# Optimization experiments

Measured on AMD Instinct MI355X. Metric: run time of the kernel, lower is better.

## Reference

```python
import jax, jax.numpy as jnp
import numpy as np

NUM_HEADS = 8
HEAD_DIM = 64  # hidden_size 512 / 8 heads


def setup_inputs() -> dict:
    key = jax.random.key(0)
    ks = jax.random.split(key, 9)
    B, S, D, H = 64, 512, 512, 512  # batch, feat_num, input_size, hidden_size
    s = 0.02
    return {
        "x": jax.random.normal(ks[0], (B, S, D), dtype=jnp.float32),
        "wq": jax.random.normal(ks[1], (D, H), dtype=jnp.float32) * s,
        "bq": jax.random.normal(ks[2], (H,), dtype=jnp.float32) * s,
        "wk": jax.random.normal(ks[3], (D, H), dtype=jnp.float32) * s,
        "bk": jax.random.normal(ks[4], (H,), dtype=jnp.float32) * s,
        "wv": jax.random.normal(ks[5], (D, H), dtype=jnp.float32) * s,
        "bv": jax.random.normal(ks[6], (H,), dtype=jnp.float32) * s,
        "wo": jax.random.normal(ks[7], (H, D), dtype=jnp.float32) * s,
        "bo": jax.random.normal(ks[8], (D,), dtype=jnp.float32) * s,
    }


def reference(x, wq, bq, wk, bk, wv, bv, wo, bo):
    B, S, D = x.shape
    # QKV projections -> [B, heads, S, head_dim]
    def split_heads(t):
        return t.reshape(B, S, NUM_HEADS, HEAD_DIM).transpose(0, 2, 1, 3)
    q = split_heads(x @ wq + bq)
    k = split_heads(x @ wk + bk)
    v = split_heads(x @ wv + bv)
    # attention: [B, h, S, S]
    scores = jnp.einsum("bhsd,bhtd->bhst", q, k) / jnp.sqrt(
        jnp.asarray(HEAD_DIM, dtype=x.dtype)
    )
    probs = jax.nn.softmax(scores, axis=-1)  # dropout p=0 -> identity
    ctx = jnp.einsum("bhst,bhtd->bhsd", probs, v)
    ctx = ctx.transpose(0, 2, 1, 3).reshape(B, S, NUM_HEADS * HEAD_DIM)
    # output dense + residual + relu (dropout identity)
    out = jax.nn.relu(x + (ctx @ wo + bo))
    return out
```

## Files before the change

kernel.cpp:

```cpp
#include <hip/hip_runtime.h>
#include <hip/hip_bf16.h>

typedef unsigned short u16;
typedef unsigned int u32;
typedef __attribute__((ext_vector_type(8))) short short8;
typedef __attribute__((ext_vector_type(4))) float f32x4;
typedef __attribute__((ext_vector_type(4))) _Float16 f16x4;

static __device__ __forceinline__ u16 f2b(float f) {
  unsigned u = __builtin_bit_cast(unsigned, f);
  unsigned r = u + 0x7fffu + ((u >> 16) & 1u);
  return (u16)(r >> 16);
}
static __device__ __forceinline__ float b2f(u16 v) {
  return __builtin_bit_cast(float, (u32)v << 16);
}
static __device__ __forceinline__ unsigned pk2(float a, float b) {
  return (unsigned)f2b(a) | ((unsigned)f2b(b) << 16);
}
static __device__ __forceinline__ u32 pkh(float a, float b) {
  return __builtin_bit_cast(u32, __builtin_amdgcn_cvt_pkrtz(a, b));
}

static __device__ __forceinline__ void gl_lds16(const u16* g, u16* l) {
  __builtin_amdgcn_global_load_lds(
      (const __attribute__((address_space(1))) unsigned*)g,
      (__attribute__((address_space(3))) unsigned*)l, 16, 0, 0);
}


__global__ __launch_bounds__(256) void prep(
    const float* __restrict__ wq, const float* __restrict__ wk,
    const float* __restrict__ wv, const float* __restrict__ wo,
    const float* __restrict__ x, u16* __restrict__ wqkv_t,
    u16* __restrict__ wo_t, u16* __restrict__ xb) {
  int t = blockIdx.x * 256 + threadIdx.x;
  if (t < 786432) {
    int n = t >> 9, k = t & 511;
    const float* w = (n < 512) ? wq : (n < 1024 ? wk : wv);
    wqkv_t[(size_t)n * 512 + k] = f2b(w[k * 512 + (n & 511)]);
  } else if (t < 1048576) {
    int j = t - 786432;
    int n = j >> 9, k = j & 511;
    wo_t[(size_t)n * 512 + k] = f2b(wo[k * 512 + n]);
  } else {
    size_t i = (size_t)(t - 1048576) * 4;
    float4 v = *reinterpret_cast<const float4*>(&x[i]);
    uint2 p;
    p.x = pk2(v.x, v.y);
    p.y = pk2(v.z, v.w);
    *reinterpret_cast<uint2*>(&xb[i]) = p;
  }
}

__global__ __launch_bounds__(256, 4) void gemm_qkv(
    const u16* __restrict__ xb, const u16* __restrict__ wt,
    const float* __restrict__ bq, const float* __restrict__ bk,
    const float* __restrict__ bv, u16* __restrict__ qkv) {
  __shared__ u16 As[128 * 64];
  __shared__ u16 Bs[128 * 64];
  const int tid = threadIdx.x;
  const int wave = tid >> 6, lane = tid & 63;
  const int wm = wave & 1, wn = wave >> 1;
  const int lr = lane & 15, lg = lane >> 4;
  const int id = blockIdx.x;
  const int xcd = id & 7, s = id >> 3;
  const int n0 = (s % 12) * 128;
  const int m0 = ((s / 12) * 8 + xcd) * 128;

  const f32x4 fz = {0.f, 0.f, 0.f, 0.f};
  f32x4 acc[4][4];
#pragma unroll
  for (int i = 0; i < 4; ++i)
#pragma unroll
    for (int j = 0; j < 4; ++j) acc[i][j] = fz;

  for (int kb = 0; kb < 512; kb += 64) {
#pragma unroll
    for (int j = 0; j < 4; ++j) {
      const int cb = (wave * 4 + j) * 64;
      const int c = cb + lane;
      const int r = c >> 3;
      const int cg = (c & 7) ^ (r & 7);
      gl_lds16(&xb[(size_t)(m0 + r) * 512 + kb + (cg << 3)], &As[cb * 8]);
      gl_lds16(&wt[(size_t)(n0 + r) * 512 + kb + (cg << 3)], &Bs[cb * 8]);
    }
    __syncthreads();
#pragma unroll
    for (int ks = 0; ks < 2; ++ks) {
      short8 af[4], bb[4];
#pragma unroll
      for (int i = 0; i < 4; ++i)
        af[i] = *reinterpret_cast<const short8*>(
            &As[(wm * 64 + i * 16 + lr) * 64 +
                (((ks * 4 + lg) ^ (lr & 7)) << 3)]);
#pragma unroll
      for (int j = 0; j < 4; ++j)
        bb[j] = *reinterpret_cast<const short8*>(
            &Bs[(wn * 64 + j * 16 + lr) * 64 +
                (((ks * 4 + lg) ^ (lr & 7)) << 3)]);
#pragma unroll
      for (int i = 0; i < 4; ++i)
#pragma unroll
        for (int j = 0; j < 4; ++j)
          acc[i][j] = __builtin_amdgcn_mfma_f32_16x16x32_bf16(
              af[i], bb[j], acc[i][j], 0, 0, 0);
    }
    __syncthreads();
  }
#pragma unroll
  for (int i = 0; i < 4; ++i) {
    const int row0 = m0 + wm * 64 + i * 16 + lg * 4;
#pragma unroll
    for (int j = 0; j < 4; ++j) {
      const int col = n0 + wn * 64 + j * 16 + lr;
      const float bias =
          (col < 512) ? bq[col] : (col < 1024 ? bk[col - 512] : bv[col - 1024]);
#pragma unroll
      for (int r = 0; r < 4; ++r) {
        float v = acc[i][j][r] + bias;
        u16 ov;
        if (col < 512)
          ov = f2b(v * 0.125f);
        else if (col < 1024)
          ov = f2b(v);
        else
          ov = __builtin_bit_cast(u16, (_Float16)v);
        qkv[(size_t)(row0 + r) * 1536 + col] = ov;
      }
    }
  }
}

__global__ __launch_bounds__(256, 3) void attn(u16* __restrict__ qkv) {
  __shared__ u16 QOs[128 * 66];
  __shared__ u16 Ks[2][64 * 64];
  __shared__ u16 VsT[2][64 * 70];

  const int tid = threadIdx.x;
  const int wave = tid >> 6, lane = tid & 63;
  const int lr = lane & 15, lg = lane >> 4;
  const int bx = blockIdx.x;
  const int xcd = bx & 7, s = bx >> 3;
  const int q0 = (s & 3) * 128;
  const int bh = (s >> 2) * 8 + xcd;
  const int b = bh >> 3, h = bh & 7;
  const size_t rowbase = (size_t)b * 512;

#pragma unroll
  for (int j = 0; j < 4; ++j) {
    const int cb = (wave * 4 + j) * 64, c = cb + lane;
    const int r = c >> 3, cg = (c & 7) ^ (r & 7);
    gl_lds16(&qkv[(rowbase + q0 + r) * 1536 + h * 64 + (cg << 3)],
             &QOs[cb * 8]);
  }
#pragma unroll
  for (int j = 0; j < 2; ++j) {
    const int cb = (wave * 2 + j) * 64, c = cb + lane;
    const int r = c >> 3, cg = (c & 7) ^ (r & 7);
    gl_lds16(&qkv[(rowbase + r) * 1536 + 512 + h * 64 + (cg << 3)],
             &Ks[0][cb * 8]);
  }
  uint4 vreg[2];
#pragma unroll
  for (int i = 0; i < 2; ++i) {
    int idx = tid + i * 256, r = idx >> 3, cg = idx & 7;
    vreg[i] = *reinterpret_cast<const uint4*>(
        &qkv[(rowbase + r) * 1536 + 1024 + h * 64 + cg * 8]);
  }
#pragma unroll
  for (int i = 0; i < 2; ++i) {
    int idx = tid + i * 256, r = idx >> 3, cg = idx & 7;
    const u16* pv = reinterpret_cast<const u16*>(&vreg[i]);
#pragma unroll
    for (int jj = 0; jj < 8; ++jj) VsT[0][(cg * 8 + jj) * 70 + r] = pv[jj];
  }
  __syncthreads();

  short8 aq[2][2];
#pragma unroll
  for (int g = 0; g < 2; ++g)
#pragma unroll
    for (int ks = 0; ks < 2; ++ks)
      aq[g][ks] = *reinterpret_cast<const short8*>(
          &QOs[(wave * 32 + g * 16 + lr) * 64 +
               (((ks * 4 + lg) ^ (lr & 7)) << 3)]);

  const f32x4 fz = {0.f, 0.f, 0.f, 0.f};
  f32x4 oacc[2][4];
#pragma unroll
  for (int g = 0; g < 2; ++g)
#pragma unroll
    for (int dt = 0; dt < 4; ++dt) oacc[g][dt] = fz;
  float lsum[2] = {0.f, 0.f};

  for (int tt = 0; tt < 8; ++tt) {
    const int buf = tt & 1;
    if (tt < 7) {
#pragma unroll
      for (int j = 0; j < 2; ++j) {
        const int cb = (wave * 2 + j) * 64, c = cb + lane;
        const int r = c >> 3, cg = (c & 7) ^ (r & 7);
        gl_lds16(&qkv[(rowbase + (tt + 1) * 64 + r) * 1536 + 512 + h * 64 +
                      (cg << 3)],
                 &Ks[buf ^ 1][cb * 8]);
      }
#pragma unroll
      for (int i = 0; i < 2; ++i) {
        int idx = tid + i * 256, r = idx >> 3, cg = idx & 7;
        vreg[i] = *reinterpret_cast<const uint4*>(
            &qkv[(rowbase + (tt + 1) * 64 + r) * 1536 + 1024 + h * 64 + cg * 8]);
      }
    }

    f32x4 st[2][4];
#pragma unroll
    for (int g = 0; g < 2; ++g)
#pragma unroll
      for (int mt = 0; mt < 4; ++mt) st[g][mt] = fz;
#pragma unroll
    for (int mt = 0; mt < 4; ++mt) {
      short8 k0 = *reinterpret_cast<const short8*>(
          &Ks[buf][(mt * 16 + lr) * 64 + ((lg ^ (lr & 7)) << 3)]);
      short8 k1 = *reinterpret_cast<const short8*>(
          &Ks[buf][(mt * 16 + lr) * 64 + (((4 + lg) ^ (lr & 7)) << 3)]);
#pragma unroll
      for (int g = 0; g < 2; ++g) {
        st[g][mt] = __builtin_amdgcn_mfma_f32_16x16x32_bf16(k0, aq[g][0],
                                                            st[g][mt], 0, 0, 0);
        st[g][mt] = __builtin_amdgcn_mfma_f32_16x16x32_bf16(k1, aq[g][1],
                                                            st[g][mt], 0, 0, 0);
      }
    }

    f16x4 pfrag[2][4];
#pragma unroll
    for (int g = 0; g < 2; ++g)
#pragma unroll
      for (int mt = 0; mt < 4; ++mt) {
        float e0 = __expf(st[g][mt][0]), e1 = __expf(st[g][mt][1]);
        float e2 = __expf(st[g][mt][2]), e3 = __expf(st[g][mt][3]);
        lsum[g] += (e0 + e1) + (e2 + e3);
        uint2 uu;
        uu.x = pkh(e0, e1);
        uu.y = pkh(e2, e3);
        pfrag[g][mt] = __builtin_bit_cast(f16x4, uu);
      }

#pragma unroll
    for (int dt = 0; dt < 4; ++dt) {
#pragma unroll
      for (int tw = 0; tw < 4; ++tw) {
        const int a0 = (dt * 16 + lr) * 70 + tw * 16 + lg * 4;
        uint2 uu;
        uu.x = *reinterpret_cast<const u32*>(&VsT[buf][a0]);
        uu.y = *reinterpret_cast<const u32*>(&VsT[buf][a0 + 2]);
        f16x4 vf = __builtin_bit_cast(f16x4, uu);
#pragma unroll
        for (int g = 0; g < 2; ++g)
          oacc[g][dt] = __builtin_amdgcn_mfma_f32_16x16x16f16(
              vf, pfrag[g][tw], oacc[g][dt], 0, 0, 0);
      }
    }

    if (tt < 7) {
#pragma unroll
      for (int i = 0; i < 2; ++i) {
        int idx = tid + i * 256, r = idx >> 3, cg = idx & 7;
        const u16* pv = reinterpret_cast<const u16*>(&vreg[i]);
#pragma unroll
        for (int jj = 0; jj < 8; ++jj)
          VsT[buf ^ 1][(cg * 8 + jj) * 70 + r] = pv[jj];
      }
    }
    __syncthreads();
  }

#pragma unroll
  for (int g = 0; g < 2; ++g) {
    float s2 = lsum[g];
    s2 += __shfl_xor(s2, 16);
    s2 += __shfl_xor(s2, 32);
    lsum[g] = 1.0f / s2;
  }
#pragma unroll
  for (int g = 0; g < 2; ++g)
#pragma unroll
    for (int dt = 0; dt < 4; ++dt) {
      f32x4 o = oacc[g][dt];
      const float li = lsum[g];
      const int base = (wave * 32 + g * 16 + lr) * 66 + dt * 16 + lg * 4;
      *reinterpret_cast<u32*>(&QOs[base]) = pk2(o[0] * li, o[1] * li);
      *reinterpret_cast<u32*>(&QOs[base + 2]) = pk2(o[2] * li, o[3] * li);
    }
  __syncthreads();
#pragma unroll
  for (int i = 0; i < 4; ++i) {
    int idx = tid + i * 256, r = idx >> 3, cg = idx & 7;
    const u16* src = &QOs[r * 66 + cg * 8];
    uint4 w;
    w.x = *reinterpret_cast<const u32*>(&src[0]);
    w.y = *reinterpret_cast<const u32*>(&src[2]);
    w.z = *reinterpret_cast<const u32*>(&src[4]);
    w.w = *reinterpret_cast<const u32*>(&src[6]);
    *reinterpret_cast<uint4*>(
        &qkv[(rowbase + q0 + r) * 1536 + h * 64 + cg * 8]) = w;
  }
}

__global__ __launch_bounds__(256, 4) void gemm_out(
    const u16* __restrict__ ctxq, const u16* __restrict__ wot,
    const u16* __restrict__ xb, const float* __restrict__ bo,
    float* __restrict__ out) {
  __shared__ u16 As[128 * 64];
  __shared__ u16 Bs[128 * 64];
  const int tid = threadIdx.x;
  const int wave = tid >> 6, lane = tid & 63;
  const int wm = wave & 1, wn = wave >> 1;
  const int lr = lane & 15, lg = lane >> 4;
  const int id = blockIdx.x;
  const int xcd = id & 7, s = id >> 3;
  const int n0 = (s & 3) * 128;
  const int m0 = ((s >> 2) * 8 + xcd) * 128;

  const f32x4 fz = {0.f, 0.f, 0.f, 0.f};
  f32x4 acc[4][4];
#pragma unroll
  for (int i = 0; i < 4; ++i)
#pragma unroll
    for (int j = 0; j < 4; ++j) acc[i][j] = fz;

  for (int kb = 0; kb < 512; kb += 64) {
#pragma unroll
    for (int j = 0; j < 4; ++j) {
      const int cb = (wave * 4 + j) * 64;
      const int c = cb + lane;
      const int r = c >> 3;
      const int cg = (c & 7) ^ (r & 7);
      gl_lds16(&ctxq[(size_t)(m0 + r) * 1536 + kb + (cg << 3)], &As[cb * 8]);
      gl_lds16(&wot[(size_t)(n0 + r) * 512 + kb + (cg << 3)], &Bs[cb * 8]);
    }
    __syncthreads();
#pragma unroll
    for (int ks = 0; ks < 2; ++ks) {
      short8 af[4], bb[4];
#pragma unroll
      for (int i = 0; i < 4; ++i)
        af[i] = *reinterpret_cast<const short8*>(
            &As[(wm * 64 + i * 16 + lr) * 64 +
                (((ks * 4 + lg) ^ (lr & 7)) << 3)]);
#pragma unroll
      for (int j = 0; j < 4; ++j)
        bb[j] = *reinterpret_cast<const short8*>(
            &Bs[(wn * 64 + j * 16 + lr) * 64 +
                (((ks * 4 + lg) ^ (lr & 7)) << 3)]);
#pragma unroll
      for (int i = 0; i < 4; ++i)
#pragma unroll
        for (int j = 0; j < 4; ++j)
          acc[i][j] = __builtin_amdgcn_mfma_f32_16x16x32_bf16(
              af[i], bb[j], acc[i][j], 0, 0, 0);
    }
    __syncthreads();
  }
#pragma unroll
  for (int i = 0; i < 4; ++i) {
#pragma unroll
    for (int j = 0; j < 4; ++j) {
      const int col = n0 + wn * 64 + j * 16 + lr;
#pragma unroll
      for (int r = 0; r < 4; ++r) {
        const int row = m0 + wm * 64 + i * 16 + lg * 4 + r;
        float v = acc[i][j][r] + bo[col] + b2f(xb[(size_t)row * 512 + col]);
        out[(size_t)row * 512 + col] = fmaxf(v, 0.0f);
      }
    }
  }
}

extern "C" void kernel_launch(void* const* d_in, const int* in_sizes, int n_in,
                              void* d_out, int out_size, void* d_ws,
                              size_t ws_size, hipStream_t stream) {
  const float* x = (const float*)d_in[0];
  const float* wq = (const float*)d_in[1];
  const float* bq = (const float*)d_in[2];
  const float* wk = (const float*)d_in[3];
  const float* bk = (const float*)d_in[4];
  const float* wv = (const float*)d_in[5];
  const float* bv = (const float*)d_in[6];
  const float* wo = (const float*)d_in[7];
  const float* bo = (const float*)d_in[8];
  float* out = (float*)d_out;

  char* ws = (char*)d_ws;
  u16* qkv = (u16*)ws;
  u16* xb = (u16*)(ws + 100663296);
  u16* wqkv_t = (u16*)(ws + 134217728);
  u16* wo_t = (u16*)(ws + 135790592);

  hipLaunchKernelGGL(prep, dim3(20480), dim3(256), 0, stream, wq, wk, wv, wo,
                     x, wqkv_t, wo_t, xb);
  hipLaunchKernelGGL(gemm_qkv, dim3(3072), dim3(256), 0, stream, xb, wqkv_t,
                     bq, bk, bv, qkv);
  hipLaunchKernelGGL(attn, dim3(2048), dim3(256), 0, stream, qkv);
  hipLaunchKernelGGL(gemm_out, dim3(1024), dim3(256), 0, stream, qkv, wo_t,
                     xb, bo, out);
}
```

Before: 277.9 us.

## Write V transposed from QKV GEMM and use bf16 32-wide MFMA for PV

The QKV GEMM epilogue now writes V in a per-batch transposed bf16 layout into a separate buffer, and Q/K into a narrower 1024-column buffer. The attention kernel loads V tiles straight into LDS with async global-to-LDS copies instead of a register round trip and scalar transposed LDS stores. P is staged through LDS as bf16 so PV can use the 16x16x32 bf16 MFMA instead of the f16 16x16x16 one. The cost is strided 8-byte stores in the GEMM epilogue, an extra LDS round trip for P, and an extra barrier.

```diff
diff --git a/kernel.cpp b/kernel.cpp
--- a/kernel.cpp
+++ b/kernel.cpp
@@ -5,7 +5,6 @@
 typedef unsigned int u32;
 typedef __attribute__((ext_vector_type(8))) short short8;
 typedef __attribute__((ext_vector_type(4))) float f32x4;
-typedef __attribute__((ext_vector_type(4))) _Float16 f16x4;
 
 static __device__ __forceinline__ u16 f2b(float f) {
   unsigned u = __builtin_bit_cast(unsigned, f);
@@ -17,9 +16,6 @@
 }
 static __device__ __forceinline__ unsigned pk2(float a, float b) {
   return (unsigned)f2b(a) | ((unsigned)f2b(b) << 16);
-}
-static __device__ __forceinline__ u32 pkh(float a, float b) {
-  return __builtin_bit_cast(u32, __builtin_amdgcn_cvt_pkrtz(a, b));
 }
 
 static __device__ __forceinline__ void gl_lds16(const u16* g, u16* l) {
@@ -56,7 +52,8 @@
 __global__ __launch_bounds__(256, 4) void gemm_qkv(
     const u16* __restrict__ xb, const u16* __restrict__ wt,
     const float* __restrict__ bq, const float* __restrict__ bk,
-    const float* __restrict__ bv, u16* __restrict__ qkv) {
+    const float* __restrict__ bv, u16* __restrict__ qkv,
+    u16* __restrict__ vT) {
   __shared__ u16 As[128 * 64];
   __shared__ u16 Bs[128 * 64];
   const int tid = threadIdx.x;
@@ -108,34 +105,44 @@
     }
     __syncthreads();
   }
-#pragma unroll
-  for (int i = 0; i < 4; ++i) {
-    const int row0 = m0 + wm * 64 + i * 16 + lg * 4;
-#pragma unroll
-    for (int j = 0; j < 4; ++j) {
-      const int col = n0 + wn * 64 + j * 16 + lr;
-      const float bias =
-          (col < 512) ? bq[col] : (col < 1024 ? bk[col - 512] : bv[col - 1024]);
-#pragma unroll
-      for (int r = 0; r < 4; ++r) {
-        float v = acc[i][j][r] + bias;
-        u16 ov;
-        if (col < 512)
-          ov = f2b(v * 0.125f);
-        else if (col < 1024)
-          ov = f2b(v);
-        else
-          ov = __builtin_bit_cast(u16, (_Float16)v);
-        qkv[(size_t)(row0 + r) * 1536 + col] = ov;
-      }
-    }
-  }
-}
-
-__global__ __launch_bounds__(256, 3) void attn(u16* __restrict__ qkv) {
-  __shared__ u16 QOs[128 * 66];
+  if (n0 < 1024) {
+#pragma unroll
+    for (int i = 0; i < 4; ++i) {
+      const int row0 = m0 + wm * 64 + i * 16 + lg * 4;
+#pragma unroll
+      for (int j = 0; j < 4; ++j) {
+        const int col = n0 + wn * 64 + j * 16 + lr;
+        const float bias = (col < 512) ? bq[col] : bk[col - 512];
+        const float sc = (col < 512) ? 0.125f : 1.0f;
+#pragma unroll
+        for (int r = 0; r < 4; ++r)
+          qkv[(size_t)(row0 + r) * 1024 + col] = f2b((acc[i][j][r] + bias) * sc);
+      }
+    }
+  } else {
+#pragma unroll
+    for (int i = 0; i < 4; ++i) {
+      const int row0 = m0 + wm * 64 + i * 16 + lg * 4;
+      const int bidx = row0 >> 9, t = row0 & 511;
+#pragma unroll
+      for (int j = 0; j < 4; ++j) {
+        const int vcol = (n0 - 1024) + wn * 64 + j * 16 + lr;
+        const float bias = bv[vcol];
+        uint2 uu;
+        uu.x = pk2(acc[i][j][0] + bias, acc[i][j][1] + bias);
+        uu.y = pk2(acc[i][j][2] + bias, acc[i][j][3] + bias);
+        *reinterpret_cast<uint2*>(
+            &vT[((size_t)bidx * 512 + vcol) * 512 + t]) = uu;
+      }
+    }
+  }
+}
+
+__global__ __launch_bounds__(256, 3) void attn(u16* __restrict__ qkv,
+                                               const u16* __restrict__ vT) {
+  __shared__ u16 PQs[128 * 72];
   __shared__ u16 Ks[2][64 * 64];
-  __shared__ u16 VsT[2][64 * 70];
+  __shared__ u16 Vs[2][64 * 64];
 
   const int tid = threadIdx.x;
   const int wave = tid >> 6, lane = tid & 63;
@@ -146,34 +153,22 @@
   const int bh = (s >> 2) * 8 + xcd;
   const int b = bh >> 3, h = bh & 7;
   const size_t rowbase = (size_t)b * 512;
+  const u16* vbase = vT + ((size_t)b * 512 + h * 64) * 512;
 
 #pragma unroll
   for (int j = 0; j < 4; ++j) {
     const int cb = (wave * 4 + j) * 64, c = cb + lane;
     const int r = c >> 3, cg = (c & 7) ^ (r & 7);
-    gl_lds16(&qkv[(rowbase + q0 + r) * 1536 + h * 64 + (cg << 3)],
-             &QOs[cb * 8]);
+    gl_lds16(&qkv[(rowbase + q0 + r) * 1024 + h * 64 + (cg << 3)],
+             &PQs[cb * 8]);
   }
 #pragma unroll
   for (int j = 0; j < 2; ++j) {
     const int cb = (wave * 2 + j) * 64, c = cb + lane;
     const int r = c >> 3, cg = (c & 7) ^ (r & 7);
-    gl_lds16(&qkv[(rowbase + r) * 1536 + 512 + h * 64 + (cg << 3)],
+    gl_lds16(&qkv[(rowbase + r) * 1024 + 512 + h * 64 + (cg << 3)],
              &Ks[0][cb * 8]);
-  }
-  uint4 vreg[2];
-#pragma unroll
-  for (int i = 0; i < 2; ++i) {
-    int idx = tid + i * 256, r = idx >> 3, cg = idx & 7;
-    vreg[i] = *reinterpret_cast<const uint4*>(
-        &qkv[(rowbase + r) * 1536 + 1024 + h * 64 + cg * 8]);
-  }
-#pragma unroll
-  for (int i = 0; i < 2; ++i) {
-    int idx = tid + i * 256, r = idx >> 3, cg = idx & 7;
-    const u16* pv = reinterpret_cast<const u16*>(&vreg[i]);
-#pragma unroll
-    for (int jj = 0; jj < 8; ++jj) VsT[0][(cg * 8 + jj) * 70 + r] = pv[jj];
+    gl_lds16(&vbase[(size_t)r * 512 + (cg << 3)], &Vs[0][cb * 8]);
   }
   __syncthreads();
 
@@ -183,8 +178,9 @@
 #pragma unroll
     for (int ks = 0; ks < 2; ++ks)
       aq[g][ks] = *reinterpret_cast<const short8*>(
-          &QOs[(wave * 32 + g * 16 + lr) * 64 +
+          &PQs[(wave * 32 + g * 16 + lr) * 64 +
                (((ks * 4 + lg) ^ (lr & 7)) << 3)]);
+  __syncthreads();
 
   const f32x4 fz = {0.f, 0.f, 0.f, 0.f};
   f32x4 oacc[2][4];
@@ -201,15 +197,11 @@
       for (int j = 0; j < 2; ++j) {
         const int cb = (wave * 2 + j) * 64, c = cb + lane;
         const int r = c >> 3, cg = (c & 7) ^ (r & 7);
-        gl_lds16(&qkv[(rowbase + (tt + 1) * 64 + r) * 1536 + 512 + h * 64 +
+        gl_lds16(&qkv[(rowbase + (tt + 1) * 64 + r) * 1024 + 512 + h * 64 +
                       (cg << 3)],
                  &Ks[buf ^ 1][cb * 8]);
-      }
-#pragma unroll
-      for (int i = 0; i < 2; ++i) {
-        int idx = tid + i * 256, r = idx >> 3, cg = idx & 7;
-        vreg[i] = *reinterpret_cast<const uint4*>(
-            &qkv[(rowbase + (tt + 1) * 64 + r) * 1536 + 1024 + h * 64 + cg * 8]);
+        gl_lds16(&vbase[(size_t)r * 512 + (tt + 1) * 64 + (cg << 3)],
+                 &Vs[buf ^ 1][cb * 8]);
       }
     }
 
@@ -233,7 +225,6 @@
       }
     }
 
-    f16x4 pfrag[2][4];
 #pragma unroll
     for (int g = 0; g < 2; ++g)
 #pragma unroll
@@ -242,35 +233,27 @@
         float e2 = __expf(st[g][mt][2]), e3 = __expf(st[g][mt][3]);
         lsum[g] += (e0 + e1) + (e2 + e3);
         uint2 uu;
-        uu.x = pkh(e0, e1);
-        uu.y = pkh(e2, e3);
-        pfrag[g][mt] = __builtin_bit_cast(f16x4, uu);
-      }
-
-#pragma unroll
-    for (int dt = 0; dt < 4; ++dt) {
-#pragma unroll
-      for (int tw = 0; tw < 4; ++tw) {
-        const int a0 = (dt * 16 + lr) * 70 + tw * 16 + lg * 4;
-        uint2 uu;
-        uu.x = *reinterpret_cast<const u32*>(&VsT[buf][a0]);
-        uu.y = *reinterpret_cast<const u32*>(&VsT[buf][a0 + 2]);
-        f16x4 vf = __builtin_bit_cast(f16x4, uu);
+        uu.x = pk2(e0, e1);
+        uu.y = pk2(e2, e3);
+        *reinterpret_cast<uint2*>(
+            &PQs[(wave * 32 + g * 16 + lr) * 72 + mt * 16 + lg * 4]) = uu;
+      }
+
+#pragma unroll
+    for (int tw = 0; tw < 2; ++tw) {
+      short8 pf[2];
+#pragma unroll
+      for (int g = 0; g < 2; ++g)
+        pf[g] = *reinterpret_cast<const short8*>(
+            &PQs[(wave * 32 + g * 16 + lr) * 72 + tw * 32 + lg * 8]);
+#pragma unroll
+      for (int dt = 0; dt < 4; ++dt) {
+        short8 vf = *reinterpret_cast<const short8*>(
+            &Vs[buf][(dt * 16 + lr) * 64 + (((tw * 4 + lg) ^ (lr & 7)) << 3)]);
 #pragma unroll
         for (int g = 0; g < 2; ++g)
-          oacc[g][dt] = __builtin_amdgcn_mfma_f32_16x16x16f16(
-              vf, pfrag[g][tw], oacc[g][dt], 0, 0, 0);
-      }
-    }
-
-    if (tt < 7) {
-#pragma unroll
-      for (int i = 0; i < 2; ++i) {
-        int idx = tid + i * 256, r = idx >> 3, cg = idx & 7;
-        const u16* pv = reinterpret_cast<const u16*>(&vreg[i]);
-#pragma unroll
-        for (int jj = 0; jj < 8; ++jj)
-          VsT[buf ^ 1][(cg * 8 + jj) * 70 + r] = pv[jj];
+          oacc[g][dt] = __builtin_amdgcn_mfma_f32_16x16x32_bf16(
+              vf, pf[g], oacc[g][dt], 0, 0, 0);
       }
     }
     __syncthreads();
@@ -290,21 +273,21 @@
       f32x4 o = oacc[g][dt];
       const float li = lsum[g];
       const int base = (wave * 32 + g * 16 + lr) * 66 + dt * 16 + lg * 4;
-      *reinterpret_cast<u32*>(&QOs[base]) = pk2(o[0] * li, o[1] * li);
-      *reinterpret_cast<u32*>(&QOs[base + 2]) = pk2(o[2] * li, o[3] * li);
+      *reinterpret_cast<u32*>(&PQs[base]) = pk2(o[0] * li, o[1] * li);
+      *reinterpret_cast<u32*>(&PQs[base + 2]) = pk2(o[2] * li, o[3] * li);
     }
   __syncthreads();
 #pragma unroll
   for (int i = 0; i < 4; ++i) {
     int idx = tid + i * 256, r = idx >> 3, cg = idx & 7;
-    const u16* src = &QOs[r * 66 + cg * 8];
+    const u16* src = &PQs[r * 66 + cg * 8];
     uint4 w;
     w.x = *reinterpret_cast<const u32*>(&src[0]);
     w.y = *reinterpret_cast<const u32*>(&src[2]);
     w.z = *reinterpret_cast<const u32*>(&src[4]);
     w.w = *reinterpret_cast<const u32*>(&src[6]);
     *reinterpret_cast<uint4*>(
-        &qkv[(rowbase + q0 + r) * 1536 + h * 64 + cg * 8]) = w;
+        &qkv[(rowbase + q0 + r) * 1024 + h * 64 + cg * 8]) = w;
   }
 }
 
@@ -337,7 +320,7 @@
       const int c = cb + lane;
       const int r = c >> 3;
       const int cg = (c & 7) ^ (r & 7);
-      gl_lds16(&ctxq[(size_t)(m0 + r) * 1536 + kb + (cg << 3)], &As[cb * 8]);
+      gl_lds16(&ctxq[(size_t)(m0 + r) * 1024 + kb + (cg << 3)], &As[cb * 8]);
       gl_lds16(&wot[(size_t)(n0 + r) * 512 + kb + (cg << 3)], &Bs[cb * 8]);
     }
     __syncthreads();
@@ -393,7 +376,8 @@
   float* out = (float*)d_out;
 
   char* ws = (char*)d_ws;
-  u16* qkv = (u16*)ws;
+  u16* qkv2 = (u16*)ws;
+  u16* vT = (u16*)(ws + 67108864);
   u16* xb = (u16*)(ws + 100663296);
   u16* wqkv_t = (u16*)(ws + 134217728);
   u16* wo_t = (u16*)(ws + 135790592);
@@ -401,8 +385,8 @@
   hipLaunchKernelGGL(prep, dim3(20480), dim3(256), 0, stream, wq, wk, wv, wo,
                      x, wqkv_t, wo_t, xb);
   hipLaunchKernelGGL(gemm_qkv, dim3(3072), dim3(256), 0, stream, xb, wqkv_t,
-                     bq, bk, bv, qkv);
-  hipLaunchKernelGGL(attn, dim3(2048), dim3(256), 0, stream, qkv);
-  hipLaunchKernelGGL(gemm_out, dim3(1024), dim3(256), 0, stream, qkv, wo_t,
+                     bq, bk, bv, qkv2, vT);
+  hipLaunchKernelGGL(attn, dim3(2048), dim3(256), 0, stream, qkv2, vT);
+  hipLaunchKernelGGL(gemm_out, dim3(1024), dim3(256), 0, stream, qkv2, wo_t,
                      xb, bo, out);
 }
```

Result: slower. 293.9 us (+5.7%).
